# Kernel tuning notes

Hardware: AMD Instinct MI355X
Metric: run time of the kernel (lower is better)

Reference implementation:

```python
import jax, jax.numpy as jnp
import numpy as np

B, T, NIN, N, NOUT = 64, 512, 64, 1024, 32
DT, TAU = 1.0, 10.0
STATE_STD, RATE_STD, OUT_STD = 0.05, 0.05, 0.05
HIDDEN_G = 1.0


def retanh(x):
    return jnp.maximum(jnp.tanh(x), 0.0)


def setup_inputs() -> dict:
    key = jax.random.key(0)
    ks = jax.random.split(key, 10)
    u = jax.random.normal(ks[0], (B, T, NIN), jnp.float32)
    x_0 = jnp.zeros((N,), jnp.float32)
    state_noise = STATE_STD * jax.random.normal(ks[1], (B, T, N), jnp.float32)
    rate_noise = RATE_STD * jax.random.normal(ks[2], (B, T, N), jnp.float32)
    output_noise = OUT_STD * jax.random.normal(ks[3], (B, T, NOUT), jnp.float32)
    W_in = jax.random.normal(ks[4], (N, NIN), jnp.float32) / np.sqrt(NIN).astype(np.float32)
    b_in = 0.1 + 0.01 * jax.random.normal(ks[5], (N,), jnp.float32)
    W_rec = jax.random.normal(ks[6], (N, N), jnp.float32) * (HIDDEN_G / np.sqrt(N).astype(np.float32))
    W_rec = W_rec * (1.0 - jnp.eye(N, dtype=jnp.float32))  # zero self-connections
    lim = 1.0 / np.sqrt(N).astype(np.float32)
    W_out = jax.random.uniform(ks[7], (NOUT, N), jnp.float32, -lim, lim)
    b_out = jax.random.uniform(ks[8], (NOUT,), jnp.float32, -lim, lim)
    return {"u": u, "x_0": x_0, "state_noise": state_noise, "rate_noise": rate_noise,
            "output_noise": output_noise, "W_in": W_in, "b_in": b_in, "W_rec": W_rec,
            "W_out": W_out, "b_out": b_out}


def reference(u, x_0, state_noise, rate_noise, output_noise, W_in, b_in, W_rec, W_out, b_out):
    alpha = DT / TAU
    # time-major for scan: [T, B, ...]
    u_t = jnp.swapaxes(u, 0, 1)
    sn = jnp.swapaxes(state_noise, 0, 1)
    rn = jnp.swapaxes(rate_noise, 0, 1)
    on = jnp.swapaxes(output_noise, 0, 1)
    x0 = jnp.broadcast_to(x_0, (B, N))
    r0 = retanh(x0)

    def step(carry, inp):
        x, r = carry
        ut, snt, rnt, ont = inp
        x_next = x + alpha * (-x + r @ W_rec.T + ut @ W_in.T + b_in + snt)
        r_next = retanh(x_next) + rnt
        z_next = r_next @ W_out.T + b_out + ont
        return (x_next, r_next), (x_next, r_next, z_next)

    _, (X, R, Z) = jax.lax.scan(step, (x0, r0), (u_t, sn, rn, on))
    # back to batch-major [B, T, ...]
    return (jnp.swapaxes(X, 0, 1), jnp.swapaxes(R, 0, 1), jnp.swapaxes(Z, 0, 1))
```

## Files before the change

kernel.cpp:

```cpp
#include <hip/hip_runtime.h>
#include <hip/hip_bf16.h>
#include <stdint.h>

#define B_    64
#define T_    512
#define NIN_  64
#define N_    1024
#define NOUT_ 32

#define NISL  16
#define BPI   16
#define MB    4
#define COLS  64
#define NT    4
#define KW    256
#define KT    8

typedef float f32x4 __attribute__((ext_vector_type(4)));
typedef short s16x8 __attribute__((ext_vector_type(8)));

__device__ __forceinline__ unsigned short f2bf(float f) {
  union { float f; unsigned u; } v; v.f = f;
  unsigned r = v.u + 0x7FFFu + ((v.u >> 16) & 1u);
  return (unsigned short)(r >> 16);
}

__device__ __forceinline__ s16x8 ld_ex16(const unsigned* p) {
  s16x8 r;
  asm volatile("global_load_dwordx4 %0, %1, off sc1"
               : "=v"(r) : "v"(p) : "memory");
  return r;
}

__global__ __launch_bounds__(256, 1) void rnn_scan(
    const float* __restrict__ U, const float* __restrict__ X0,
    const float* __restrict__ SN, const float* __restrict__ RN,
    const float* __restrict__ Wi, const float* __restrict__ Bi,
    const float* __restrict__ Wr,
    float* __restrict__ X, float* __restrict__ R,
    unsigned* __restrict__ flags, unsigned* __restrict__ ex)
{
  const int bid   = blockIdx.x;
  const int isl   = bid / BPI, slice = bid % BPI;
  const int tid   = threadIdx.x;
  const int wave  = tid >> 6, lane = tid & 63;
  const int l15   = lane & 15, koct = lane >> 4;
  const int colbase = slice * COLS;

  s16x8 bfrag[KT][NT];
#pragma unroll
  for (int kt = 0; kt < KT; ++kt) {
    const int k0 = wave * KW + kt * 32 + koct * 8;
#pragma unroll
    for (int nt = 0; nt < NT; ++nt) {
      const float* p = Wr + (size_t)(colbase + nt * 16 + l15) * N_ + k0;
      s16x8 f;
#pragma unroll
      for (int i = 0; i < 8; ++i) f[i] = (short)f2bf(p[i]);
      bfrag[kt][nt] = f;
    }
  }
  s16x8 wifrag[NT];
  if (wave < 2) {
#pragma unroll
    for (int nt = 0; nt < NT; ++nt) {
      const float* p = Wi + (size_t)(colbase + nt * 16 + l15) * NIN_ + wave * 32 + koct * 8;
      s16x8 f;
#pragma unroll
      for (int i = 0; i < 8; ++i) f[i] = (short)f2bf(p[i]);
      wifrag[nt] = f;
    }
  }

  const int cc  = lane;
  const int bloc = wave;
  const int bg  = isl * MB + bloc;
  const int nn  = colbase + cc;
  const int abatch = isl * MB + (l15 & (MB - 1));

  float x = X0[nn];
  const float bin = Bi[nn];
  const float r0 = fmaxf(tanhf(x), 0.f);

  __shared__ float part[4][COLS][MB];

  unsigned* const myflags = flags + isl * (T_ + 1);

  {
    unsigned short h = f2bf(r0);
    unsigned other = __shfl_xor((unsigned)h, 1);
    if ((lane & 1) == 0)
      __hip_atomic_store(ex + (size_t)bg * (N_ / 2) + (nn >> 1),
                         (unsigned)h | (other << 16),
                         __ATOMIC_RELAXED, __HIP_MEMORY_SCOPE_AGENT);
  }
  __syncthreads();
  if (tid == 0)
    __hip_atomic_fetch_add(myflags, 1u, __ATOMIC_RELAXED, __HIP_MEMORY_SCOPE_AGENT);

  float pxn = 0.f, prv = 0.f;

  for (int t = 0; t < T_; ++t) {
    const int par = t & 1;
    const size_t row = (size_t)bg * T_ + t;

    const float snv = SN[row * N_ + nn];
    const float rnv = RN[row * N_ + nn];
    s16x8 ua;
    if (wave < 2) {
      const float* p = U + ((size_t)(isl * MB + (l15 & (MB - 1))) * T_ + t) * NIN_
                         + wave * 32 + koct * 8;
#pragma unroll
      for (int i = 0; i < 8; ++i) ua[i] = (short)f2bf(p[i]);
    }

    while (__hip_atomic_load(myflags + t, __ATOMIC_RELAXED, __HIP_MEMORY_SCOPE_AGENT) < BPI)
      __builtin_amdgcn_s_sleep(2);

    if (t > 0) {
      X[(row - 1) * N_ + nn] = pxn;
      R[(row - 1) * N_ + nn] = prv;
    }

    const unsigned* exr = ex + (size_t)par * (B_ * (N_ / 2))
                             + (size_t)abatch * (N_ / 2);
    s16x8 afr[KT];
#pragma unroll
    for (int kt = 0; kt < KT; ++kt)
      afr[kt] = ld_ex16(exr + ((wave * KW + kt * 32 + koct * 8) >> 1));
    asm volatile("s_waitcnt vmcnt(0)" ::: "memory");
    __builtin_amdgcn_sched_barrier(0);

    f32x4 acc[NT];
#pragma unroll
    for (int nt = 0; nt < NT; ++nt) acc[nt] = f32x4{0.f, 0.f, 0.f, 0.f};
#pragma unroll
    for (int kt = 0; kt < KT; ++kt)
#pragma unroll
      for (int nt = 0; nt < NT; ++nt)
        acc[nt] = __builtin_amdgcn_mfma_f32_16x16x32_bf16(afr[kt], bfrag[kt][nt], acc[nt], 0, 0, 0);
    if (wave < 2) {
#pragma unroll
      for (int nt = 0; nt < NT; ++nt)
        acc[nt] = __builtin_amdgcn_mfma_f32_16x16x32_bf16(ua, wifrag[nt], acc[nt], 0, 0, 0);
    }

    if (lane < 16) {
#pragma unroll
      for (int nt = 0; nt < NT; ++nt)
        *(f32x4*)&part[wave][nt * 16 + lane][0] = acc[nt];
    }
    __syncthreads();
    const float mat = part[0][cc][bloc] + part[1][cc][bloc] +
                      part[2][cc][bloc] + part[3][cc][bloc];
    const float xn = x + 0.1f * (-x + mat + bin + snv);
    const float rv = fmaxf(tanhf(xn), 0.f) + rnv;
    x = xn;

    {
      unsigned short h = f2bf(rv);
      unsigned other = __shfl_xor((unsigned)h, 1);
      if ((lane & 1) == 0)
        __hip_atomic_store(ex + (size_t)(par ^ 1) * (B_ * (N_ / 2)) +
                               (size_t)bg * (N_ / 2) + (nn >> 1),
                           (unsigned)h | (other << 16),
                           __ATOMIC_RELAXED, __HIP_MEMORY_SCOPE_AGENT);
    }
    __syncthreads();
    if (tid == 0)
      __hip_atomic_fetch_add(myflags + t + 1, 1u, __ATOMIC_RELAXED, __HIP_MEMORY_SCOPE_AGENT);

    pxn = xn; prv = rv;
  }
  {
    const size_t lrow = (size_t)bg * T_ + (T_ - 1);
    X[lrow * N_ + nn] = pxn;
    R[lrow * N_ + nn] = prv;
  }
}

#define TCH 128
__global__ __launch_bounds__(256, 1) void rnn_zout(
    const float* __restrict__ Rm, const float* __restrict__ ON,
    const float* __restrict__ Wo, const float* __restrict__ Bo,
    float* __restrict__ Z)
{
  const int bid = blockIdx.x;
  const int b = bid >> 2, tq = bid & 3;
  const int tid = threadIdx.x;
  const int o = tid & 31, kc = tid >> 5;

  float4 wv[32];
  const float4* wp = (const float4*)(Wo + (size_t)o * N_ + kc * 128);
#pragma unroll
  for (int i = 0; i < 32; ++i) wv[i] = wp[i];

  __shared__ float Rl[N_];
  __shared__ float zred[8][32];

  for (int t = tq * TCH; t < tq * TCH + TCH; ++t) {
    const size_t row = (size_t)b * T_ + t;
    ((float4*)Rl)[tid] = ((const float4*)(Rm + row * N_))[tid];
    __syncthreads();
    float a0 = 0.f;
#pragma unroll
    for (int i = 0; i < 32; ++i) {
      const float* rp = Rl + kc * 128 + i * 4;
      a0 += wv[i].x * rp[0] + wv[i].y * rp[1] + wv[i].z * rp[2] + wv[i].w * rp[3];
    }
    zred[kc][o] = a0;
    __syncthreads();
    if (tid < 32) {
      float z = Bo[tid];
#pragma unroll
      for (int k = 0; k < 8; ++k) z += zred[k][tid];
      Z[row * NOUT_ + tid] = z + ON[row * NOUT_ + tid];
    }
  }
}

extern "C" void kernel_launch(void* const* d_in, const int* in_sizes, int n_in,
                              void* d_out, int out_size, void* d_ws, size_t ws_size,
                              hipStream_t stream) {
  const float* U  = (const float*)d_in[0];
  const float* X0 = (const float*)d_in[1];
  const float* SN = (const float*)d_in[2];
  const float* RN = (const float*)d_in[3];
  const float* ON = (const float*)d_in[4];
  const float* Wi = (const float*)d_in[5];
  const float* Bi = (const float*)d_in[6];
  const float* Wr = (const float*)d_in[7];
  const float* Wo = (const float*)d_in[8];
  const float* Bo = (const float*)d_in[9];

  float* X = (float*)d_out;
  float* R = X + (size_t)B_ * T_ * N_;
  float* Z = R + (size_t)B_ * T_ * N_;

  unsigned* flags = (unsigned*)d_ws;
  unsigned* ex    = (unsigned*)((char*)d_ws + 65536);

  hipMemsetAsync(flags, 0, NISL * (T_ + 1) * sizeof(unsigned), stream);

  hipLaunchKernelGGL(rnn_scan, dim3(NISL * BPI), dim3(256), 0, stream,
                     U, X0, SN, RN, Wi, Bi, Wr, X, R, flags, ex);
  hipLaunchKernelGGL(rnn_zout, dim3(B_ * (T_ / TCH)), dim3(256), 0, stream,
                     R, ON, Wo, Bo, Z);
}
```

Measured before the change: 1.583 ms.

## Replace flag-counter barrier with tag bits embedded in exchanged bf16 data

Removes the per-step flag counter, block-wide sync and atomic increment. Readiness is now signalled by a parity tag stored in the low bit of each exchanged bf16 word, and readers spin-reload until every word carries the expected tag. The change also prefetches noise two steps ahead, vectorises weight and input conversion, swizzles the shared partial-sum layout to avoid bank conflicts, and writes X/R directly each step. It trades one bf16 mantissa bit for the tag and relies on the memset to 0xFF for the initial tag state.

Result: slower. 2.050 ms (+29.5%).

```diff
diff --git a/kernel.cpp b/kernel.cpp
--- a/kernel.cpp
+++ b/kernel.cpp
@@ -16,6 +16,8 @@
 #define KW    256
 #define KT    8
 
+#define EX_WORDS (2 * B_ * (N_ / 2))
+
 typedef float f32x4 __attribute__((ext_vector_type(4)));
 typedef short s16x8 __attribute__((ext_vector_type(8)));
 
@@ -25,12 +27,24 @@
   return (unsigned short)(r >> 16);
 }
 
-__device__ __forceinline__ s16x8 ld_ex16(const unsigned* p) {
-  s16x8 r;
-  asm volatile("global_load_dwordx4 %0, %1, off sc1"
-               : "=v"(r) : "v"(p) : "memory");
-  return r;
-}
+__device__ __forceinline__ s16x8 cvt8(float4 a, float4 b) {
+  s16x8 f;
+  f[0] = (short)f2bf(a.x); f[1] = (short)f2bf(a.y);
+  f[2] = (short)f2bf(a.z); f[3] = (short)f2bf(a.w);
+  f[4] = (short)f2bf(b.x); f[5] = (short)f2bf(b.y);
+  f[6] = (short)f2bf(b.z); f[7] = (short)f2bf(b.w);
+  return f;
+}
+
+#define LD16(dst, base, OFF) \
+  asm volatile("global_load_dwordx4 %0, %1, off offset:" #OFF " sc0 sc1" \
+               : "=v"(dst) : "v"(base) : "memory")
+
+#define LDALL() do { \
+  LD16(afr[0], bp, 0);   LD16(afr[1], bp, 64);  \
+  LD16(afr[2], bp, 128); LD16(afr[3], bp, 192); \
+  LD16(afr[4], bp, 256); LD16(afr[5], bp, 320); \
+  LD16(afr[6], bp, 384); LD16(afr[7], bp, 448); } while (0)
 
 __global__ __launch_bounds__(256, 1) void rnn_scan(
     const float* __restrict__ U, const float* __restrict__ X0,
@@ -38,7 +52,7 @@
     const float* __restrict__ Wi, const float* __restrict__ Bi,
     const float* __restrict__ Wr,
     float* __restrict__ X, float* __restrict__ R,
-    unsigned* __restrict__ flags, unsigned* __restrict__ ex)
+    unsigned* __restrict__ ex)
 {
   const int bid   = blockIdx.x;
   const int isl   = bid / BPI, slice = bid % BPI;
@@ -53,83 +67,83 @@
     const int k0 = wave * KW + kt * 32 + koct * 8;
 #pragma unroll
     for (int nt = 0; nt < NT; ++nt) {
-      const float* p = Wr + (size_t)(colbase + nt * 16 + l15) * N_ + k0;
-      s16x8 f;
-#pragma unroll
-      for (int i = 0; i < 8; ++i) f[i] = (short)f2bf(p[i]);
-      bfrag[kt][nt] = f;
+      const float4* q = (const float4*)(Wr + (size_t)(colbase + nt * 16 + l15) * N_ + k0);
+      bfrag[kt][nt] = cvt8(q[0], q[1]);
     }
   }
   s16x8 wifrag[NT];
   if (wave < 2) {
 #pragma unroll
     for (int nt = 0; nt < NT; ++nt) {
-      const float* p = Wi + (size_t)(colbase + nt * 16 + l15) * NIN_ + wave * 32 + koct * 8;
-      s16x8 f;
-#pragma unroll
-      for (int i = 0; i < 8; ++i) f[i] = (short)f2bf(p[i]);
-      wifrag[nt] = f;
-    }
-  }
-
-  const int cc  = lane;
+      const float4* q = (const float4*)(Wi + (size_t)(colbase + nt * 16 + l15) * NIN_ + wave * 32 + koct * 8);
+      wifrag[nt] = cvt8(q[0], q[1]);
+    }
+  }
+
+  const int cc   = lane;
   const int bloc = wave;
-  const int bg  = isl * MB + bloc;
-  const int nn  = colbase + cc;
-  const int abatch = isl * MB + (l15 & (MB - 1));
-
-  float x = X0[nn];
+  const int bg   = isl * MB + bloc;
+  const int nn   = colbase + cc;
+  const int abatch = isl * MB + (l15 & 3);
+  const int ub   = isl * MB + (l15 & 3);
+
+  const float* SNp = SN + (size_t)bg * T_ * N_ + nn;
+  const float* RNp = RN + (size_t)bg * T_ * N_ + nn;
+  float*       Xp  = X  + (size_t)bg * T_ * N_ + nn;
+  float*       Rp  = R  + (size_t)bg * T_ * N_ + nn;
+  const float* Up  = U  + (size_t)ub * T_ * NIN_ + wave * 32 + koct * 8;
+
+  const int kbase_dw = (wave * KW + koct * 8) >> 1;
+  const unsigned* ex0 = ex + (size_t)abatch * (N_ / 2) + kbase_dw;
+  const unsigned* ex1 = ex0 + (size_t)B_ * (N_ / 2);
+  unsigned* exw0 = ex + (size_t)bg * (N_ / 2) + (nn >> 1);
+  unsigned* exw1 = exw0 + (size_t)B_ * (N_ / 2);
+
+  const float x0v = X0[nn];
   const float bin = Bi[nn];
-  const float r0 = fmaxf(tanhf(x), 0.f);
+  float sn_c = SNp[0], rn_c = RNp[0];
+  float sn_n = SNp[N_], rn_n = RNp[N_];
 
   __shared__ float part[4][COLS][MB];
 
-  unsigned* const myflags = flags + isl * (T_ + 1);
-
   {
+    const float r0 = fmaxf(tanhf(x0v), 0.f);
     unsigned short h = f2bf(r0);
     unsigned other = __shfl_xor((unsigned)h, 1);
-    if ((lane & 1) == 0)
-      __hip_atomic_store(ex + (size_t)bg * (N_ / 2) + (nn >> 1),
-                         (unsigned)h | (other << 16),
-                         __ATOMIC_RELAXED, __HIP_MEMORY_SCOPE_AGENT);
-  }
-  __syncthreads();
-  if (tid == 0)
-    __hip_atomic_fetch_add(myflags, 1u, __ATOMIC_RELAXED, __HIP_MEMORY_SCOPE_AGENT);
-
-  float pxn = 0.f, prv = 0.f;
-
+    if (!(lane & 1)) {
+      unsigned vv = ((unsigned)h & ~1u) | (other << 16);
+      __hip_atomic_store(exw0, vv, __ATOMIC_RELAXED, __HIP_MEMORY_SCOPE_AGENT);
+    }
+  }
+
+  float x = x0v;
   for (int t = 0; t < T_; ++t) {
-    const int par = t & 1;
-    const size_t row = (size_t)bg * T_ + t;
-
-    const float snv = SN[row * N_ + nn];
-    const float rnv = RN[row * N_ + nn];
-    s16x8 ua;
+    const unsigned tgm = ((t >> 1) & 1) ? 0xFFFFFFFFu : 0u;
+    const unsigned* bp = (t & 1) ? ex1 : ex0;
+
+    float4 uq0, uq1;
     if (wave < 2) {
-      const float* p = U + ((size_t)(isl * MB + (l15 & (MB - 1))) * T_ + t) * NIN_
-                         + wave * 32 + koct * 8;
-#pragma unroll
-      for (int i = 0; i < 8; ++i) ua[i] = (short)f2bf(p[i]);
-    }
-
-    while (__hip_atomic_load(myflags + t, __ATOMIC_RELAXED, __HIP_MEMORY_SCOPE_AGENT) < BPI)
-      __builtin_amdgcn_s_sleep(2);
-
-    if (t > 0) {
-      X[(row - 1) * N_ + nn] = pxn;
-      R[(row - 1) * N_ + nn] = prv;
-    }
-
-    const unsigned* exr = ex + (size_t)par * (B_ * (N_ / 2))
-                             + (size_t)abatch * (N_ / 2);
+      const float4* q = (const float4*)(Up + (size_t)t * NIN_);
+      uq0 = q[0]; uq1 = q[1];
+    }
+
     s16x8 afr[KT];
-#pragma unroll
-    for (int kt = 0; kt < KT; ++kt)
-      afr[kt] = ld_ex16(exr + ((wave * KW + kt * 32 + koct * 8) >> 1));
-    asm volatile("s_waitcnt vmcnt(0)" ::: "memory");
+    LDALL();
+    for (;;) {
+      asm volatile("s_waitcnt vmcnt(0)" ::: "memory");
+      unsigned bad = 0;
+#pragma unroll
+      for (int kt = 0; kt < KT; ++kt) {
+        union { s16x8 v; unsigned u[4]; } w; w.v = afr[kt];
+        bad |= (w.u[0] ^ tgm) | (w.u[1] ^ tgm) | (w.u[2] ^ tgm) | (w.u[3] ^ tgm);
+      }
+      if (__all((int)((bad & 1u) == 0u))) break;
+      LDALL();
+    }
     __builtin_amdgcn_sched_barrier(0);
+
+    float sn2 = 0.f, rn2 = 0.f;
+    if (t + 2 < T_) { sn2 = SNp[(size_t)(t + 2) * N_]; rn2 = RNp[(size_t)(t + 2) * N_]; }
 
     f32x4 acc[NT];
 #pragma unroll
@@ -140,6 +154,7 @@
       for (int nt = 0; nt < NT; ++nt)
         acc[nt] = __builtin_amdgcn_mfma_f32_16x16x32_bf16(afr[kt], bfrag[kt][nt], acc[nt], 0, 0, 0);
     if (wave < 2) {
+      s16x8 ua = cvt8(uq0, uq1);
 #pragma unroll
       for (int nt = 0; nt < NT; ++nt)
         acc[nt] = __builtin_amdgcn_mfma_f32_16x16x32_bf16(ua, wifrag[nt], acc[nt], 0, 0, 0);
@@ -147,35 +162,36 @@
 
     if (lane < 16) {
 #pragma unroll
-      for (int nt = 0; nt < NT; ++nt)
-        *(f32x4*)&part[wave][nt * 16 + lane][0] = acc[nt];
+      for (int nt = 0; nt < NT; ++nt) {
+        const int s = (nt * 2 + (lane >> 3)) & 3;
+        f32x4 a = acc[nt];
+        if (s & 1) a = f32x4{a[1], a[0], a[3], a[2]};
+        if (s & 2) a = f32x4{a[2], a[3], a[0], a[1]};
+        *(f32x4*)&part[wave][nt * 16 + lane][0] = a;
+      }
     }
     __syncthreads();
-    const float mat = part[0][cc][bloc] + part[1][cc][bloc] +
-                      part[2][cc][bloc] + part[3][cc][bloc];
-    const float xn = x + 0.1f * (-x + mat + bin + snv);
-    const float rv = fmaxf(tanhf(xn), 0.f) + rnv;
+    const int sr = (cc >> 3) & 3;
+    const float mat = part[0][cc][bloc ^ sr] + part[1][cc][bloc ^ sr] +
+                      part[2][cc][bloc ^ sr] + part[3][cc][bloc ^ sr];
+    const float xn = x + 0.1f * (-x + mat + bin + sn_c);
+    const float rv = fmaxf(tanhf(xn), 0.f) + rn_c;
     x = xn;
 
     {
+      const unsigned tgn = ((t + 1) >> 1) & 1;
       unsigned short h = f2bf(rv);
       unsigned other = __shfl_xor((unsigned)h, 1);
-      if ((lane & 1) == 0)
-        __hip_atomic_store(ex + (size_t)(par ^ 1) * (B_ * (N_ / 2)) +
-                               (size_t)bg * (N_ / 2) + (nn >> 1),
-                           (unsigned)h | (other << 16),
+      if (!(lane & 1)) {
+        unsigned vv = (((unsigned)h & ~1u) | tgn) | (other << 16);
+        __hip_atomic_store((t & 1) ? exw0 : exw1, vv,
                            __ATOMIC_RELAXED, __HIP_MEMORY_SCOPE_AGENT);
-    }
-    __syncthreads();
-    if (tid == 0)
-      __hip_atomic_fetch_add(myflags + t + 1, 1u, __ATOMIC_RELAXED, __HIP_MEMORY_SCOPE_AGENT);
-
-    pxn = xn; prv = rv;
-  }
-  {
-    const size_t lrow = (size_t)bg * T_ + (T_ - 1);
-    X[lrow * N_ + nn] = pxn;
-    R[lrow * N_ + nn] = prv;
+      }
+    }
+    Xp[(size_t)t * N_] = xn;
+    Rp[(size_t)t * N_] = rv;
+
+    sn_c = sn_n; rn_c = rn_n; sn_n = sn2; rn_n = rn2;
   }
 }
 
@@ -237,13 +253,12 @@
   float* R = X + (size_t)B_ * T_ * N_;
   float* Z = R + (size_t)B_ * T_ * N_;
 
-  unsigned* flags = (unsigned*)d_ws;
-  unsigned* ex    = (unsigned*)((char*)d_ws + 65536);
-
-  hipMemsetAsync(flags, 0, NISL * (T_ + 1) * sizeof(unsigned), stream);
+  unsigned* ex = (unsigned*)d_ws;
+
+  hipMemsetAsync(ex, 0xFF, EX_WORDS * sizeof(unsigned), stream);
 
   hipLaunchKernelGGL(rnn_scan, dim3(NISL * BPI), dim3(256), 0, stream,
-                     U, X0, SN, RN, Wi, Bi, Wr, X, R, flags, ex);
+                     U, X0, SN, RN, Wi, Bi, Wr, X, R, ex);
   hipLaunchKernelGGL(rnn_zout, dim3(B_ * (T_ / TCH)), dim3(256), 0, stream,
                      R, ON, Wo, Bo, Z);
 }
```
